# Kernel tuning notes

Hardware: AMD Instinct MI355X
Metric: run time of the kernel (lower is better)

The kernel has to match this reference:

```python
import jax, jax.numpy as jnp
import numpy as np

B, S, H = 8, 8192, 1024
CAPACITY_FACTOR = 0.5


def setup_inputs() -> dict:
    key = jax.random.key(0)
    ks = jax.random.split(key, 5)
    sc = lambda fan: np.float32(1.0 / np.sqrt(fan))
    return {
        "x": jax.random.normal(ks[0], (B, S, H), dtype=jnp.float32),
        # router: Linear(H, H//4) -> ReLU -> Linear(H//4, 1)
        "W1": jax.random.normal(ks[1], (H, H // 4), dtype=jnp.float32) * sc(H),
        "b1": jnp.zeros((H // 4,), dtype=jnp.float32),
        "W2": jax.random.normal(ks[2], (H // 4, 1), dtype=jnp.float32) * sc(H // 4),
        "b2": jnp.zeros((1,), dtype=jnp.float32),
        # external layer_fn realized as a dense layer: gelu(x @ Wl)
        "Wl": jax.random.normal(ks[3], (H, H), dtype=jnp.float32) * sc(H),
    }


def reference(x, W1, b1, W2, b2, Wl):
    # router scores [B, S, 1]
    scores = jax.nn.relu(jnp.einsum("bsh,hd->bsd", x, W1) + b1)
    scores = jnp.einsum("bsd,do->bso", scores, W2) + b2
    routing_weights = jax.nn.sigmoid(scores)  # [B, S, 1]

    # eval path: process only top-capacity tokens per batch row
    capacity = int(S * CAPACITY_FACTOR)
    _, top_idx = jax.lax.top_k(scores[..., 0], capacity)  # [B, C]

    selected = jnp.take_along_axis(x, top_idx[..., None], axis=1)  # [B, C, H]
    processed = jax.nn.gelu(jnp.einsum("bch,hd->bcd", selected, Wl))  # layer_fn

    batch_idx = jnp.arange(x.shape[0])[:, None]  # [B, 1]
    output = x.at[batch_idx, top_idx].set(processed)  # scatter back into clone of x
    return output, routing_weights
```

## Files before the change

### kernel.cpp

```cpp
#include <hip/hip_runtime.h>
#include <stdint.h>

#define B_   8
#define S_   8192
#define H_   1024
#define HQ_  256
#define CAP_ 4096
#define UCAP_ (S_-CAP_)
#define M_   (B_*CAP_)
#define EPSB 0.012f
#define LCAP 8192

using f32x4 = __attribute__((ext_vector_type(4))) float;
using s16x8 = __attribute__((ext_vector_type(8))) short;

__device__ __forceinline__ unsigned short f2bf(float f) {
  unsigned u = __float_as_uint(f);
  u += 0x7FFF + ((u >> 16) & 1);
  return (unsigned short)(u >> 16);
}
__device__ __forceinline__ float bf2f(unsigned short h) {
  return __uint_as_float(((unsigned)h) << 16);
}

__device__ __forceinline__ float gelu_f(float v) {
  float s = v + 0.044715f * v * v * v;
  float e = __expf(-1.5957691216057308f * s);
  return v * __builtin_amdgcn_rcpf(1.0f + e);
}

__device__ __forceinline__ unsigned mono(float f) {
  unsigned u = __float_as_uint(f);
  return (u & 0x80000000u) ? ~u : (u | 0x80000000u);
}
__device__ __forceinline__ float unmono(unsigned k) {
  unsigned u = (k & 0x80000000u) ? (k & 0x7fffffffu) : ~k;
  return __uint_as_float(u);
}

__device__ __forceinline__ void gload_lds16(const void* g, void* l) {
  __builtin_amdgcn_global_load_lds(
      (const __attribute__((address_space(1))) void*)(uintptr_t)g,
      (__attribute__((address_space(3))) void*)(uintptr_t)l,
      16, 0, 0);
}

__device__ __forceinline__ int swz4(int row) {
  return (row & 3) ^ ((row >> 2) & 3);
}

__global__ __launch_bounds__(256) void prep_w1_kernel(
    const float* __restrict__ W1, unsigned short* __restrict__ w1t_hi) {
  __shared__ float tile[32][33];
  const int n0 = blockIdx.x * 32, k0 = blockIdx.y * 32;
  const int tx = threadIdx.x, ty = threadIdx.y;
  for (int i = ty; i < 32; i += 8) tile[i][tx] = W1[(size_t)(k0 + i) * HQ_ + n0 + tx];
  __syncthreads();
  for (int i = ty; i < 32; i += 8)
    w1t_hi[(size_t)(n0 + i) * H_ + k0 + tx] = f2bf(tile[tx][i]);
}

__global__ __launch_bounds__(512) void router_mfma_kernel(
    const float* __restrict__ x, const unsigned short* __restrict__ w1t_hi,
    const float* __restrict__ b1, const float* __restrict__ W2,
    const float* __restrict__ b2, float* __restrict__ scores,
    float* __restrict__ rw) {
  __shared__ __align__(16) unsigned short AsH[2][128 * 32];
  __shared__ __align__(16) unsigned short BsH[2][256 * 32];
  __shared__ float part[128][4];
  const int t = threadIdx.x;
  const int lane = t & 63, w = t >> 6;
  const int m0 = blockIdx.x * 128;
  const int wr = w >> 2, wc = w & 3;
  const int r16 = lane & 15, ks = lane >> 4;

  const float* aptr[2];
  int aso[2];
  #pragma unroll
  for (int u = 0; u < 2; ++u) {
    int idx = t + u * 512;
    int row = idx >> 3, q = idx & 7;
    aptr[u] = x + (size_t)(m0 + row) * H_ + q * 4;
    aso[u] = row * 32 + (((q >> 1) ^ swz4(row)) << 3) + (q & 1) * 4;
  }
  const unsigned short* bptr[2];
  int bdst[2];
  #pragma unroll
  for (int u = 0; u < 2; ++u) {
    int c = u * 512 + t;
    int row = c >> 2, sl = c & 3;
    int slz = sl ^ swz4(row);
    bptr[u] = w1t_hi + (size_t)row * H_ + slz * 8;
    bdst[u] = (u * 512 + w * 64) * 8;
  }

  f32x4 acc[4][4];
  #pragma unroll
  for (int i = 0; i < 4; ++i)
    #pragma unroll
    for (int j = 0; j < 4; ++j) acc[i][j] = (f32x4){0.f, 0.f, 0.f, 0.f};

  {
    #pragma unroll
    for (int u = 0; u < 2; ++u) gload_lds16(bptr[u], &BsH[0][bdst[u]]);
    float4 av[2];
    #pragma unroll
    for (int u = 0; u < 2; ++u) av[u] = *(const float4*)(aptr[u]);
    #pragma unroll
    for (int u = 0; u < 2; ++u) {
      ushort4 hh;
      hh.x = f2bf(av[u].x); hh.y = f2bf(av[u].y);
      hh.z = f2bf(av[u].z); hh.w = f2bf(av[u].w);
      *(ushort4*)&AsH[0][aso[u]] = hh;
    }
    __syncthreads();
  }

  for (int kt = 0; kt < 32; ++kt) {
    const int cur = kt & 1, nxt = cur ^ 1;
    const int k1 = (kt + 1) * 32;
    const bool pf = (kt < 31);
    float4 av[2];
    if (pf) {
      #pragma unroll
      for (int u = 0; u < 2; ++u) gload_lds16(bptr[u] + k1, &BsH[nxt][bdst[u]]);
      #pragma unroll
      for (int u = 0; u < 2; ++u) av[u] = *(const float4*)(aptr[u] + k1);
    }
    s16x8 ah[4], bh[4];
    #pragma unroll
    for (int i = 0; i < 4; ++i) {
      int r = wr * 64 + i * 16 + r16;
      ah[i] = *(const s16x8*)&AsH[cur][r * 32 + (ks ^ swz4(r)) * 8];
    }
    #pragma unroll
    for (int j = 0; j < 4; ++j) {
      int r = wc * 64 + j * 16 + r16;
      bh[j] = *(const s16x8*)&BsH[cur][r * 32 + (ks ^ swz4(r)) * 8];
    }
    #pragma unroll
    for (int i = 0; i < 4; ++i)
      #pragma unroll
      for (int j = 0; j < 4; ++j)
        acc[i][j] = __builtin_amdgcn_mfma_f32_16x16x32_bf16(ah[i], bh[j], acc[i][j], 0, 0, 0);
    if (pf) {
      __builtin_amdgcn_sched_barrier(0);
      #pragma unroll
      for (int u = 0; u < 2; ++u) {
        ushort4 hh;
        hh.x = f2bf(av[u].x); hh.y = f2bf(av[u].y);
        hh.z = f2bf(av[u].z); hh.w = f2bf(av[u].w);
        *(ushort4*)&AsH[nxt][aso[u]] = hh;
      }
    }
    asm volatile("s_waitcnt lgkmcnt(0)" ::: "memory");
    __builtin_amdgcn_s_barrier();
    __builtin_amdgcn_sched_barrier(0);
  }

  float b1v[4], w2v[4];
  #pragma unroll
  for (int j = 0; j < 4; ++j) {
    int n = wc * 64 + j * 16 + r16;
    b1v[j] = b1[n]; w2v[j] = W2[n];
  }
  const int g4 = lane >> 4;
  #pragma unroll
  for (int i = 0; i < 4; ++i) {
    #pragma unroll
    for (int r = 0; r < 4; ++r) {
      float p = 0.f;
      #pragma unroll
      for (int j = 0; j < 4; ++j) {
        float h = acc[i][j][r] + b1v[j];
        h = fmaxf(h, 0.f);
        p = fmaf(h, w2v[j], p);
      }
      p += __shfl_xor(p, 1);
      p += __shfl_xor(p, 2);
      p += __shfl_xor(p, 4);
      p += __shfl_xor(p, 8);
      if (r16 == 0) part[wr * 64 + i * 16 + g4 * 4 + r][wc] = p;
    }
  }
  __syncthreads();
  if (t < 128) {
    float sc = part[t][0] + part[t][1] + part[t][2] + part[t][3] + b2[0];
    scores[m0 + t] = sc;
    rw[m0 + t] = 1.f / (1.f + expf(-sc));
  }
}

__global__ __launch_bounds__(1024) void select_kernel(
    const float* __restrict__ scores, float* __restrict__ thr) {
  __shared__ unsigned hist[2048];
  __shared__ unsigned sh_b, sh_gt;
  const int b = blockIdx.x;
  const int tid = threadIdx.x;
  const float* srow = scores + (size_t)b * S_;
  unsigned prefix = 0; int plen = 0; unsigned rank = CAP_;
  #pragma unroll
  for (int round = 0; round < 3; ++round) {
    const int nb = (round < 2) ? 11 : 10;
    hist[tid] = 0; hist[tid + 1024] = 0;
    __syncthreads();
    for (int i = tid; i < S_; i += 1024) {
      unsigned k = mono(srow[i]);
      if (plen == 0 || (k >> (32 - plen)) == prefix) {
        unsigned bucket = (k << plen) >> (32 - nb);
        atomicAdd(&hist[bucket], 1u);
      }
    }
    __syncthreads();
    for (int s = 1; s < 2048; s <<= 1) {
      unsigned t0 = (tid + s < 2048) ? hist[tid + s] : 0;
      unsigned t1 = (tid + 1024 + s < 2048) ? hist[tid + 1024 + s] : 0;
      __syncthreads();
      hist[tid] += t0; hist[tid + 1024] += t1;
      __syncthreads();
    }
    #pragma unroll
    for (int h = 0; h < 2; ++h) {
      int i = tid + h * 1024;
      unsigned ge = hist[i];
      unsigned gt = (i < 2047) ? hist[i + 1] : 0;
      if (gt < rank && rank <= ge) { sh_b = (unsigned)i; sh_gt = gt; }
    }
    __syncthreads();
    prefix = (prefix << nb) | sh_b;
    plen += nb;
    rank -= sh_gt;
    __syncthreads();
  }
  if (tid == 0) thr[b] = unmono(prefix);
}

__global__ __launch_bounds__(256) void band_kernel(
    const float* __restrict__ scores, const float* __restrict__ thr,
    int* __restrict__ list, int* __restrict__ count) {
  int i = blockIdx.x * 256 + threadIdx.x;
  float s = scores[i];
  int b = i >> 13;
  if (fabsf(s - thr[b]) <= EPSB) {
    int p = atomicAdd(count, 1);
    if (p < LCAP) list[p] = i;
  }
}

__global__ __launch_bounds__(256) void recompute_kernel(
    const float* __restrict__ x, const float* __restrict__ W1,
    const float* __restrict__ b1, const float* __restrict__ W2,
    const float* __restrict__ b2, const int* __restrict__ list,
    const int* __restrict__ count, float* __restrict__ scores,
    float* __restrict__ rw) {
  __shared__ float xr[4][H_];
  __shared__ float red[4][4];
  int n = *count; if (n > LCAP) n = LCAP;
  const int j = threadIdx.x;
  for (int base = blockIdx.x * 4; base < n; base += gridDim.x * 4) {
    int nt = n - base; if (nt > 4) nt = 4;
    for (int tt = 0; tt < 4; ++tt) {
      int tok = list[base + ((tt < nt) ? tt : 0)];
      const float* xrow = x + (size_t)tok * H_;
      for (int k = j; k < H_; k += 256) xr[tt][k] = xrow[k];
    }
    __syncthreads();
    float a0 = 0.f, a1 = 0.f, a2 = 0.f, a3 = 0.f;
    for (int k = 0; k < H_; ++k) {
      float wv = W1[(size_t)k * HQ_ + j];
      a0 = fmaf(xr[0][k], wv, a0);
      a1 = fmaf(xr[1][k], wv, a1);
      a2 = fmaf(xr[2][k], wv, a2);
      a3 = fmaf(xr[3][k], wv, a3);
    }
    float aa[4] = {a0, a1, a2, a3};
    #pragma unroll
    for (int tt = 0; tt < 4; ++tt) {
      float h = fmaxf(aa[tt] + b1[j], 0.f);
      float v = h * W2[j];
      v += __shfl_xor(v, 1);  v += __shfl_xor(v, 2);  v += __shfl_xor(v, 4);
      v += __shfl_xor(v, 8);  v += __shfl_xor(v, 16); v += __shfl_xor(v, 32);
      if ((j & 63) == 0) red[tt][j >> 6] = v;
    }
    __syncthreads();
    if (j < nt) {
      int tok = list[base + j];
      float sc = red[j][0] + red[j][1] + red[j][2] + red[j][3] + b2[0];
      scores[tok] = sc;
      rw[tok] = 1.f / (1.f + expf(-sc));
    }
    __syncthreads();
  }
}

__global__ __launch_bounds__(1024) void compact_kernel(
    const float* __restrict__ scores, const float* __restrict__ thr,
    int* __restrict__ comp, int* __restrict__ ucomp) {
  __shared__ int wc_eq[16], wc_sel[16], red[16];
  const int b = blockIdx.x;
  const float T = thr[b];
  const float* srow = scores + (size_t)b * S_;
  const int tid = threadIdx.x, lane = tid & 63, wid = tid >> 6;

  int cgt = 0;
  #pragma unroll
  for (int c = 0; c < 8; ++c) cgt += (srow[c * 1024 + tid] > T) ? 1 : 0;
  cgt += __shfl_xor(cgt, 1);  cgt += __shfl_xor(cgt, 2);  cgt += __shfl_xor(cgt, 4);
  cgt += __shfl_xor(cgt, 8);  cgt += __shfl_xor(cgt, 16); cgt += __shfl_xor(cgt, 32);
  if (lane == 0) red[wid] = cgt;
  __syncthreads();
  int cnt_gt = 0;
  #pragma unroll
  for (int i = 0; i < 16; ++i) cnt_gt += red[i];
  const int need = CAP_ - cnt_gt;

  int* crow = comp + b * CAP_;
  int* urow = ucomp + b * UCAP_;
  int sel_base = 0, unsel_base = 0, eq_base = 0;
  __syncthreads();
  for (int c = 0; c < 8; ++c) {
    int idx = c * 1024 + tid;
    float s = srow[idx];
    bool gt = s > T, eq = (s == T);
    unsigned long long meq = __ballot(eq);
    if (lane == 0) wc_eq[wid] = __popcll(meq);
    __syncthreads();
    int eq_off = eq_base, eq_tot = 0;
    #pragma unroll
    for (int w2 = 0; w2 < 16; ++w2) { if (w2 < wid) eq_off += wc_eq[w2]; eq_tot += wc_eq[w2]; }
    int eqpos = eq_off + __popcll(meq & ((1ull << lane) - 1));
    bool take = gt || (eq && eqpos < need);
    unsigned long long mt = __ballot(take);
    if (lane == 0) wc_sel[wid] = __popcll(mt);
    __syncthreads();
    int sel_off = sel_base, sel_tot = 0;
    #pragma unroll
    for (int w2 = 0; w2 < 16; ++w2) { if (w2 < wid) sel_off += wc_sel[w2]; sel_tot += wc_sel[w2]; }
    if (take) {
      crow[sel_off + __popcll(mt & ((1ull << lane) - 1))] = idx;
    } else {
      int un_off = unsel_base + wid * 64 - (sel_off - sel_base);
      urow[un_off + __popcll(~mt & ((1ull << lane) - 1))] = idx;
    }
    sel_base += sel_tot; unsel_base += 1024 - sel_tot; eq_base += eq_tot;
    __syncthreads();
  }
}

__global__ __launch_bounds__(256) void copy_unsel_kernel(
    const float* __restrict__ x, const int* __restrict__ ucomp,
    float* __restrict__ out) {
  int i = blockIdx.x;
  int b = i >> 12, r = i & (UCAP_ - 1);
  int token = ucomp[b * UCAP_ + r];
  size_t row = (size_t)b * S_ + token;
  const float4* src = (const float4*)(x + row * H_);
  float4* dst = (float4*)(out + row * H_);
  dst[threadIdx.x] = src[threadIdx.x];
}

__global__ __launch_bounds__(256) void wlt_kernel(
    const float* __restrict__ wl, unsigned short* __restrict__ wlt) {
  __shared__ float tile[32][33];
  const int x0 = blockIdx.x * 32, y0 = blockIdx.y * 32;
  const int tx = threadIdx.x, ty = threadIdx.y;
  for (int i = ty; i < 32; i += 8) tile[i][tx] = wl[(size_t)(y0 + i) * H_ + x0 + tx];
  __syncthreads();
  for (int i = ty; i < 32; i += 8)
    wlt[(size_t)(x0 + i) * H_ + y0 + tx] = f2bf(tile[tx][i]);
}

__global__ __launch_bounds__(256) void gather_cast_kernel(
    const float* __restrict__ x, const int* __restrict__ comp,
    unsigned short* __restrict__ xg) {
  int tid = blockIdx.x * 256 + threadIdx.x;
  int rowc = tid >> 8;
  int c4 = tid & 255;
  int b = rowc >> 12, cc = rowc & (CAP_ - 1);
  int token = comp[b * CAP_ + cc];
  float4 v = *(const float4*)&x[((size_t)(b * S_ + token)) * H_ + c4 * 4];
  ushort4 o;
  o.x = f2bf(v.x); o.y = f2bf(v.y); o.z = f2bf(v.z); o.w = f2bf(v.w);
  *(ushort4*)&xg[(size_t)rowc * H_ + c4 * 4] = o;
}

__global__ __launch_bounds__(256) void moe_gemm_kernel(
    const unsigned short* __restrict__ xg, const unsigned short* __restrict__ wlt,
    const int* __restrict__ comp, float* __restrict__ out) {
  __shared__ __align__(16) unsigned short As[2][128 * 32];
  __shared__ __align__(16) unsigned short Bs[2][128 * 32];
  __shared__ int toks[128];
  const int t = threadIdx.x;
  const int lane = t & 63, w = t >> 6;
  const int bid = blockIdx.x;
  const int xcd = bid & 7, wl_ = bid >> 3;
  const int m0 = (xcd * 32 + (wl_ >> 3)) * 128;
  const int n0 = (wl_ & 7) * 128;
  const int bb = m0 >> 12;
  if (t < 128) toks[t] = comp[bb * CAP_ + (m0 & (CAP_ - 1)) + t];
  const int wr = w >> 1, wc = w & 1;
  const int r16 = lane & 15, ks = lane >> 4;

  const unsigned short *aP[2], *bP[2];
  int dst[2];
  #pragma unroll
  for (int u = 0; u < 2; ++u) {
    int c = u * 256 + t;
    int row = c >> 2, sl = c & 3;
    int slz = sl ^ swz4(row);
    aP[u] = xg + (size_t)(m0 + row) * H_ + slz * 8;
    bP[u] = wlt + (size_t)(n0 + row) * H_ + slz * 8;
    dst[u] = (u * 256 + w * 64) * 8;
  }

  f32x4 acc[4][4];
  #pragma unroll
  for (int i = 0; i < 4; ++i)
    #pragma unroll
    for (int j = 0; j < 4; ++j) acc[i][j] = (f32x4){0.f, 0.f, 0.f, 0.f};

  #pragma unroll
  for (int u = 0; u < 2; ++u) {
    gload_lds16(aP[u], &As[0][dst[u]]);
    gload_lds16(bP[u], &Bs[0][dst[u]]);
  }
  asm volatile("s_waitcnt vmcnt(0)" ::: "memory");
  __builtin_amdgcn_s_barrier();
  __builtin_amdgcn_sched_barrier(0);

  for (int kt = 0; kt < 32; ++kt) {
    const int cur = kt & 1;
    const int k1 = (kt + 1) * 32;
    if (kt < 31) {
      #pragma unroll
      for (int u = 0; u < 2; ++u) {
        gload_lds16(aP[u] + k1, &As[cur ^ 1][dst[u]]);
        gload_lds16(bP[u] + k1, &Bs[cur ^ 1][dst[u]]);
      }
      asm volatile("s_waitcnt vmcnt(4)" ::: "memory");
    } else {
      asm volatile("s_waitcnt vmcnt(0)" ::: "memory");
    }
    __builtin_amdgcn_s_barrier();
    __builtin_amdgcn_sched_barrier(0);
    s16x8 af[4], bfr[4];
    #pragma unroll
    for (int i = 0; i < 4; ++i) {
      int r = wr * 64 + i * 16 + r16;
      af[i] = *(const s16x8*)&As[cur][r * 32 + (ks ^ swz4(r)) * 8];
    }
    #pragma unroll
    for (int j = 0; j < 4; ++j) {
      int r = wc * 64 + j * 16 + r16;
      bfr[j] = *(const s16x8*)&Bs[cur][r * 32 + (ks ^ swz4(r)) * 8];
    }
    #pragma unroll
    for (int i = 0; i < 4; ++i)
      #pragma unroll
      for (int j = 0; j < 4; ++j)
        acc[i][j] = __builtin_amdgcn_mfma_f32_16x16x32_bf16(af[i], bfr[j], acc[i][j], 0, 0, 0);
    __builtin_amdgcn_s_barrier();
    __builtin_amdgcn_sched_barrier(0);
  }

  #pragma unroll
  for (int i = 0; i < 4; ++i) {
    #pragma unroll
    for (int r = 0; r < 4; ++r) {
      int rl = wr * 64 + i * 16 + (lane >> 4) * 4 + r;
      int token = toks[rl];
      float* orow = out + ((size_t)(bb * S_ + token)) * H_ + n0 + wc * 64;
      #pragma unroll
      for (int j = 0; j < 4; ++j)
        orow[j * 16 + r16] = gelu_f(acc[i][j][r]);
    }
  }
}

extern "C" void kernel_launch(void* const* d_in, const int* in_sizes, int n_in,
                              void* d_out, int out_size, void* d_ws, size_t ws_size,
                              hipStream_t stream) {
  const float* x  = (const float*)d_in[0];
  const float* W1 = (const float*)d_in[1];
  const float* b1 = (const float*)d_in[2];
  const float* W2 = (const float*)d_in[3];
  const float* b2 = (const float*)d_in[4];
  const float* Wl = (const float*)d_in[5];
  float* out = (float*)d_out;
  float* rw  = out + (size_t)B_ * S_ * H_;

  char* ws = (char*)d_ws;
  float* scores        = (float*)ws;
  int*   comp          = (int*)(ws + (256 << 10));
  float* thr           = (float*)(ws + (384 << 10));
  int*   count         = (int*)(ws + (384 << 10) + 256);
  int*   list          = (int*)(ws + (384 << 10) + 512);
  int*   ucomp         = (int*)(ws + (448 << 10));
  unsigned short* wlt  = (unsigned short*)(ws + (1 << 20));
  unsigned short* xg   = (unsigned short*)(ws + (3 << 20));
  unsigned short* w1t_hi = xg;

  hipMemsetAsync(count, 0, sizeof(int), stream);
  hipLaunchKernelGGL(prep_w1_kernel, dim3(HQ_/32, H_/32), dim3(32, 8), 0, stream,
                     W1, w1t_hi);
  hipLaunchKernelGGL(router_mfma_kernel, dim3((B_*S_)/128), dim3(512), 0, stream,
                     x, w1t_hi, b1, W2, b2, scores, rw);
  hipLaunchKernelGGL(select_kernel, dim3(B_), dim3(1024), 0, stream, scores, thr);
  hipLaunchKernelGGL(band_kernel, dim3((B_*S_)/256), dim3(256), 0, stream,
                     scores, thr, list, count);
  hipLaunchKernelGGL(recompute_kernel, dim3(128), dim3(256), 0, stream,
                     x, W1, b1, W2, b2, list, count, scores, rw);
  hipLaunchKernelGGL(select_kernel, dim3(B_), dim3(1024), 0, stream, scores, thr);
  hipLaunchKernelGGL(compact_kernel, dim3(B_), dim3(1024), 0, stream,
                     scores, thr, comp, ucomp);
  hipLaunchKernelGGL(copy_unsel_kernel, dim3(B_*UCAP_), dim3(256), 0, stream,
                     x, ucomp, out);
  hipLaunchKernelGGL(wlt_kernel, dim3(H_/32, H_/32), dim3(32, 8), 0, stream, Wl, wlt);
  hipLaunchKernelGGL(gather_cast_kernel, dim3(M_*H_/4/256), dim3(256), 0, stream,
                     x, comp, xg);
  hipLaunchKernelGGL(moe_gemm_kernel, dim3((M_/128)*(H_/128)), dim3(256), 0, stream,
                     xg, wlt, comp, out);
}
```

Baseline: 427.3 us.

## Deepen router and MoE GEMM pipelines to triple-buffered prefetch two tiles ahead

Both the router GEMM and the capacity-token GEMM move from double-buffered LDS staging to a three-stage ring. Global loads now run two K-tiles ahead. The MoE GEMM also drops one of its two barriers per iteration. The aim is to hide more global-memory latency behind MFMA work, at the cost of more LDS per block (which may lower occupancy) and more in-flight registers in the router, where the fp32 A tile is held in registers two stages deep.

```diff
diff --git a/kernel.cpp b/kernel.cpp
--- a/kernel.cpp
+++ b/kernel.cpp
@@ -66,7 +66,7 @@
     const float* __restrict__ b2, float* __restrict__ scores,
     float* __restrict__ rw) {
   __shared__ __align__(16) unsigned short AsH[2][128 * 32];
-  __shared__ __align__(16) unsigned short BsH[2][256 * 32];
+  __shared__ __align__(16) unsigned short BsH[3][256 * 32];
   __shared__ float part[128][4];
   const int t = threadIdx.x;
   const int lane = t & 63, w = t >> 6;
@@ -100,63 +100,86 @@
     #pragma unroll
     for (int j = 0; j < 4; ++j) acc[i][j] = (f32x4){0.f, 0.f, 0.f, 0.f};
 
+  float4 av[2][2];
+
   {
+    float4 a0[2];
+    #pragma unroll
+    for (int u = 0; u < 2; ++u) a0[u] = *(const float4*)(aptr[u]);
     #pragma unroll
     for (int u = 0; u < 2; ++u) gload_lds16(bptr[u], &BsH[0][bdst[u]]);
-    float4 av[2];
-    #pragma unroll
-    for (int u = 0; u < 2; ++u) av[u] = *(const float4*)(aptr[u]);
     #pragma unroll
     for (int u = 0; u < 2; ++u) {
       ushort4 hh;
-      hh.x = f2bf(av[u].x); hh.y = f2bf(av[u].y);
-      hh.z = f2bf(av[u].z); hh.w = f2bf(av[u].w);
+      hh.x = f2bf(a0[u].x); hh.y = f2bf(a0[u].y);
+      hh.z = f2bf(a0[u].z); hh.w = f2bf(a0[u].w);
       *(ushort4*)&AsH[0][aso[u]] = hh;
     }
-    __syncthreads();
-  }
-
-  for (int kt = 0; kt < 32; ++kt) {
-    const int cur = kt & 1, nxt = cur ^ 1;
-    const int k1 = (kt + 1) * 32;
-    const bool pf = (kt < 31);
-    float4 av[2];
-    if (pf) {
-      #pragma unroll
-      for (int u = 0; u < 2; ++u) gload_lds16(bptr[u] + k1, &BsH[nxt][bdst[u]]);
-      #pragma unroll
-      for (int u = 0; u < 2; ++u) av[u] = *(const float4*)(aptr[u] + k1);
-    }
-    s16x8 ah[4], bh[4];
-    #pragma unroll
-    for (int i = 0; i < 4; ++i) {
-      int r = wr * 64 + i * 16 + r16;
-      ah[i] = *(const s16x8*)&AsH[cur][r * 32 + (ks ^ swz4(r)) * 8];
-    }
-    #pragma unroll
-    for (int j = 0; j < 4; ++j) {
-      int r = wc * 64 + j * 16 + r16;
-      bh[j] = *(const s16x8*)&BsH[cur][r * 32 + (ks ^ swz4(r)) * 8];
-    }
-    #pragma unroll
-    for (int i = 0; i < 4; ++i)
-      #pragma unroll
-      for (int j = 0; j < 4; ++j)
-        acc[i][j] = __builtin_amdgcn_mfma_f32_16x16x32_bf16(ah[i], bh[j], acc[i][j], 0, 0, 0);
-    if (pf) {
-      __builtin_amdgcn_sched_barrier(0);
-      #pragma unroll
-      for (int u = 0; u < 2; ++u) {
-        ushort4 hh;
-        hh.x = f2bf(av[u].x); hh.y = f2bf(av[u].y);
-        hh.z = f2bf(av[u].z); hh.w = f2bf(av[u].w);
-        *(ushort4*)&AsH[nxt][aso[u]] = hh;
-      }
-    }
+    #pragma unroll
+    for (int u = 0; u < 2; ++u) av[1][u] = *(const float4*)(aptr[u] + 32);
+    #pragma unroll
+    for (int u = 0; u < 2; ++u) gload_lds16(bptr[u] + 32, &BsH[1][bdst[u]]);
+    asm volatile("s_waitcnt vmcnt(4)" ::: "memory");
     asm volatile("s_waitcnt lgkmcnt(0)" ::: "memory");
     __builtin_amdgcn_s_barrier();
     __builtin_amdgcn_sched_barrier(0);
   }
+
+  int bcur = 0, bstage = 2;
+
+#define RSTEP(KT, SI, SC) do {                                                  \
+    const int kt_ = (KT);                                                       \
+    if (kt_ <= 29) {                                                            \
+      _Pragma("unroll")                                                         \
+      for (int u = 0; u < 2; ++u)                                               \
+        av[SI][u] = *(const float4*)(aptr[u] + (kt_ + 2) * 32);                 \
+      _Pragma("unroll")                                                         \
+      for (int u = 0; u < 2; ++u)                                               \
+        gload_lds16(bptr[u] + (kt_ + 2) * 32, &BsH[bstage][bdst[u]]);           \
+    }                                                                           \
+    {                                                                           \
+      s16x8 ah[4], bh[4];                                                       \
+      _Pragma("unroll")                                                         \
+      for (int i = 0; i < 4; ++i) {                                             \
+        int r = wr * 64 + i * 16 + r16;                                         \
+        ah[i] = *(const s16x8*)&AsH[kt_ & 1][r * 32 + (ks ^ swz4(r)) * 8];      \
+      }                                                                         \
+      _Pragma("unroll")                                                         \
+      for (int j = 0; j < 4; ++j) {                                             \
+        int r = wc * 64 + j * 16 + r16;                                         \
+        bh[j] = *(const s16x8*)&BsH[bcur][r * 32 + (ks ^ swz4(r)) * 8];         \
+      }                                                                         \
+      _Pragma("unroll")                                                         \
+      for (int i = 0; i < 4; ++i)                                               \
+        _Pragma("unroll")                                                       \
+        for (int j = 0; j < 4; ++j)                                             \
+          acc[i][j] = __builtin_amdgcn_mfma_f32_16x16x32_bf16(ah[i], bh[j],     \
+                                                              acc[i][j], 0,0,0);\
+    }                                                                           \
+    __builtin_amdgcn_sched_barrier(0);                                          \
+    if (kt_ <= 30) {                                                            \
+      _Pragma("unroll")                                                         \
+      for (int u = 0; u < 2; ++u) {                                             \
+        ushort4 hh;                                                             \
+        hh.x = f2bf(av[SC][u].x); hh.y = f2bf(av[SC][u].y);                     \
+        hh.z = f2bf(av[SC][u].z); hh.w = f2bf(av[SC][u].w);                     \
+        *(ushort4*)&AsH[(kt_ + 1) & 1][aso[u]] = hh;                            \
+      }                                                                         \
+    }                                                                           \
+    if (kt_ <= 29)      asm volatile("s_waitcnt vmcnt(4)" ::: "memory");        \
+    else if (kt_ == 30) asm volatile("s_waitcnt vmcnt(0)" ::: "memory");        \
+    asm volatile("s_waitcnt lgkmcnt(0)" ::: "memory");                          \
+    __builtin_amdgcn_s_barrier();                                               \
+    __builtin_amdgcn_sched_barrier(0);                                          \
+    bcur = (bcur == 2) ? 0 : bcur + 1;                                          \
+    bstage = (bstage == 2) ? 0 : bstage + 1;                                    \
+  } while (0)
+
+  for (int kk2 = 0; kk2 < 32; kk2 += 2) {
+    RSTEP(kk2, 0, 1);
+    RSTEP(kk2 + 1, 1, 0);
+  }
+#undef RSTEP
 
   float b1v[4], w2v[4];
   #pragma unroll
@@ -387,8 +410,8 @@
 __global__ __launch_bounds__(256) void moe_gemm_kernel(
     const unsigned short* __restrict__ xg, const unsigned short* __restrict__ wlt,
     const int* __restrict__ comp, float* __restrict__ out) {
-  __shared__ __align__(16) unsigned short As[2][128 * 32];
-  __shared__ __align__(16) unsigned short Bs[2][128 * 32];
+  __shared__ __align__(16) unsigned short As[3][128 * 32];
+  __shared__ __align__(16) unsigned short Bs[3][128 * 32];
   __shared__ int toks[128];
   const int t = threadIdx.x;
   const int lane = t & 63, w = t >> 6;
@@ -424,43 +447,50 @@
     gload_lds16(aP[u], &As[0][dst[u]]);
     gload_lds16(bP[u], &Bs[0][dst[u]]);
   }
-  asm volatile("s_waitcnt vmcnt(0)" ::: "memory");
+  #pragma unroll
+  for (int u = 0; u < 2; ++u) {
+    gload_lds16(aP[u] + 32, &As[1][dst[u]]);
+    gload_lds16(bP[u] + 32, &Bs[1][dst[u]]);
+  }
+  asm volatile("s_waitcnt vmcnt(4)" ::: "memory");
   __builtin_amdgcn_s_barrier();
   __builtin_amdgcn_sched_barrier(0);
 
+  int bcur = 0, bstage = 2;
   for (int kt = 0; kt < 32; ++kt) {
-    const int cur = kt & 1;
-    const int k1 = (kt + 1) * 32;
-    if (kt < 31) {
+    if (kt <= 29) {
+      const int k2 = (kt + 2) * 32;
       #pragma unroll
       for (int u = 0; u < 2; ++u) {
-        gload_lds16(aP[u] + k1, &As[cur ^ 1][dst[u]]);
-        gload_lds16(bP[u] + k1, &Bs[cur ^ 1][dst[u]]);
+        gload_lds16(aP[u] + k2, &As[bstage][dst[u]]);
+        gload_lds16(bP[u] + k2, &Bs[bstage][dst[u]]);
       }
-      asm volatile("s_waitcnt vmcnt(4)" ::: "memory");
-    } else {
-      asm volatile("s_waitcnt vmcnt(0)" ::: "memory");
-    }
+    }
+    {
+      s16x8 af[4], bfr[4];
+      #pragma unroll
+      for (int i = 0; i < 4; ++i) {
+        int r = wr * 64 + i * 16 + r16;
+        af[i] = *(const s16x8*)&As[bcur][r * 32 + (ks ^ swz4(r)) * 8];
+      }
+      #pragma unroll
+      for (int j = 0; j < 4; ++j) {
+        int r = wc * 64 + j * 16 + r16;
+        bfr[j] = *(const s16x8*)&Bs[bcur][r * 32 + (ks ^ swz4(r)) * 8];
+      }
+      #pragma unroll
+      for (int i = 0; i < 4; ++i)
+        #pragma unroll
+        for (int j = 0; j < 4; ++j)
+          acc[i][j] = __builtin_amdgcn_mfma_f32_16x16x32_bf16(af[i], bfr[j], acc[i][j], 0, 0, 0);
+    }
+    __builtin_amdgcn_sched_barrier(0);
+    if (kt <= 29)      asm volatile("s_waitcnt vmcnt(4)" ::: "memory");
+    else if (kt == 30) asm volatile("s_waitcnt vmcnt(0)" ::: "memory");
     __builtin_amdgcn_s_barrier();
     __builtin_amdgcn_sched_barrier(0);
-    s16x8 af[4], bfr[4];
-    #pragma unroll
-    for (int i = 0; i < 4; ++i) {
-      int r = wr * 64 + i * 16 + r16;
-      af[i] = *(const s16x8*)&As[cur][r * 32 + (ks ^ swz4(r)) * 8];
-    }
-    #pragma unroll
-    for (int j = 0; j < 4; ++j) {
-      int r = wc * 64 + j * 16 + r16;
-      bfr[j] = *(const s16x8*)&Bs[cur][r * 32 + (ks ^ swz4(r)) * 8];
-    }
-    #pragma unroll
-    for (int i = 0; i < 4; ++i)
-      #pragma unroll
-      for (int j = 0; j < 4; ++j)
-        acc[i][j] = __builtin_amdgcn_mfma_f32_16x16x32_bf16(af[i], bfr[j], acc[i][j], 0, 0, 0);
-    __builtin_amdgcn_s_barrier();
-    __builtin_amdgcn_sched_barrier(0);
+    bcur = (bcur == 2) ? 0 : bcur + 1;
+    bstage = (bstage == 2) ? 0 : bstage + 1;
   }
 
   #pragma unroll
```

Result: no change. 435.6 us (+2.0%).
